# Optimization experiments

Measured on AMD Instinct MI355X. Metric: run time of the kernel, lower is better.

Reference implementation:

```python
import jax, jax.numpy as jnp
import numpy as np
import math

B, N, K, H = 128, 39, 10, 256
RATIO = 0.8
K1 = math.ceil(RATIO * N)    # 32
K2 = math.ceil(RATIO * K1)   # 26
K3 = math.ceil(RATIO * K2)   # 21


def _edge_conv(x_flat, nb, n, w, b):
    # DynamicEdgeConv: per-graph kNN on features (self included, as torch_cluster.knn),
    # message = relu(Linear([x_i, x_j - x_i])), max aggregation over the K neighbors.
    f = x_flat.shape[-1]
    x = x_flat.reshape(nb, n, f)
    sq = jnp.sum(x * x, axis=-1)                                   # [nb,n]
    d = sq[:, :, None] + sq[:, None, :] - 2.0 * jnp.einsum('bif,bjf->bij', x, x)
    _, idx = jax.lax.top_k(-d, K)                                  # [nb,n,K] nearest
    xj = x[jnp.arange(nb)[:, None, None], idx]                     # [nb,n,K,f]
    xi = x[:, :, None, :]
    msg = jnp.concatenate([jnp.broadcast_to(xi, xj.shape), xj - xi], axis=-1)
    h = jax.nn.relu(msg @ w + b)
    return jnp.max(h, axis=2).reshape(nb * n, -1)


def _gcn_score(x_flat, adj, w, b):
    # GCNConv(in,1) with self-loops + symmetric normalization (SAGPool score layer)
    nb, n, _ = adj.shape
    x = x_flat.reshape(nb, n, -1)
    a = adj + jnp.eye(n, dtype=adj.dtype)
    dinv = jax.lax.rsqrt(jnp.sum(a, axis=-1))
    an = a * dinv[:, :, None] * dinv[:, None, :]
    s = jnp.einsum('bij,bjf->bif', an, x @ w) + b
    return s[..., 0]                                               # [nb,n]


def _sag_pool(x_flat, adj, k, w, b):
    # SAGPool: GCN score, per-graph top-k, gate kept nodes by tanh(score), filter adj.
    nb, n, _ = adj.shape
    score = _gcn_score(x_flat, adj, w, b)
    top, loc = jax.lax.top_k(score, k)                             # [nb,k]
    bi = jnp.arange(nb)[:, None]
    x = x_flat.reshape(nb, n, -1)
    xp = x[bi, loc] * jnp.tanh(top)[..., None]
    adj_p = adj[jnp.arange(nb)[:, None, None], loc[:, :, None], loc[:, None, :]]
    perm = (bi * n + loc).reshape(-1)                              # flat node ids
    return xp.reshape(nb * k, -1), adj_p, perm


def _bn(x, g, b, eps=1e-5):
    m = jnp.mean(x, axis=0)
    v = jnp.var(x, axis=0)
    return (x - m) * jax.lax.rsqrt(v + eps) * g + b


def _readout(x_flat, nb, k):
    x = x_flat.reshape(nb, k, -1)
    return jnp.concatenate([jnp.max(x, axis=1), jnp.mean(x, axis=1)], axis=1)


def reference(x, adj, w_mlp1, b_mlp1, w_mlp2, b_mlp2, w_mlp3, b_mlp3, w_mlp6, b_mlp6,
              bn1_g, bn1_b, bn2_g, bn2_b, bn3_g, bn3_b,
              p1_w, p1_b, p2_w, p2_b, p3_w, p3_b,
              lin1_w, lin1_b, lin2_w, lin2_b, lin3_w, lin3_b,
              lin4_w, lin4_b, lin5_w, lin5_b, lin6_w, lin6_b):
    relu = jax.nn.relu
    deg_gt = jnp.sum(adj, axis=-1).reshape(B * N)                  # degree(edge_index[0])

    def decoder(xf):
        d = jnp.tanh(_edge_conv(xf, B, N, w_mlp3, b_mlp3))         # conv4
        d = jnp.tanh(_edge_conv(d, B, N, w_mlp2, b_mlp2))          # conv5
        return _edge_conv(d, B, N, w_mlp6, b_mlp6)                 # conv6

    def degree_head(xf):
        h = relu(xf @ lin4_w + lin4_b)
        h = relu(h @ lin5_w + lin5_b)
        return relu(h @ lin6_w + lin6_b)

    # ---- level 1 ----
    h1 = relu(_bn(_edge_conv(x.reshape(B * N, N), B, N, w_mlp1, b_mlp1), bn1_g, bn1_b))
    xp1, adj1, perm1 = _sag_pool(h1, adj, K1, p1_w, p1_b)
    x_out1 = jnp.zeros_like(h1).at[perm1].set(xp1)
    x_dec1 = decoder(x_out1)
    x_degree = degree_head(x_out1)   # source reuses this tensor for levels 2/3 preds
    gt1, pred1 = deg_gt[perm1], x_degree[perm1]
    r1 = _readout(xp1, B, K1)

    # ---- level 2 ----
    h2 = relu(_bn(_edge_conv(xp1, B, K1, w_mlp2, b_mlp2), bn2_g, bn2_b))
    xp2, adj2, perm2 = _sag_pool(h2, adj1, K2, p2_w, p2_b)
    inner2 = jnp.zeros_like(h2).at[perm2].set(xp2)
    x_out2 = jnp.zeros_like(h1).at[perm1].set(inner2)
    x_dec2 = decoder(x_out2)
    gt2, pred2 = deg_gt[perm2], x_degree[perm2]
    r2 = _readout(xp2, B, K2)

    # ---- level 3 ----
    h3 = relu(_bn(_edge_conv(xp2, B, K2, w_mlp3, b_mlp3), bn3_g, bn3_b))
    xp3, adj3, perm3 = _sag_pool(h3, adj2, K3, p3_w, p3_b)
    inner3 = jnp.zeros_like(h3).at[perm3].set(xp3)
    x_out3 = jnp.zeros_like(h1).at[perm2].set(inner3)  # faithful: source uses perm_2 here
    x_dec3 = decoder(x_out3)
    gt3, pred3 = deg_gt[perm3], x_degree[perm3]
    r3 = _readout(xp3, B, K3)

    z = r1 + r2 + r3
    z = relu(z @ lin1_w + lin1_b)
    z = relu(z @ lin2_w + lin2_b)
    probs = jax.nn.softmax(z @ lin3_w + lin3_b, axis=1)
    return (probs, x_dec1, x_dec2, x_dec3, gt1, pred1, gt2, pred2, gt3, pred3)


def setup_inputs() -> dict:
    key = jax.random.key(0)
    ks = jax.random.split(key, 32)
    rn = lambda i, shape: jax.random.normal(ks[i], shape, dtype=jnp.float32) * 0.05
    x = jax.random.normal(ks[0], (B, N, N), dtype=jnp.float32)
    adj = (jax.random.uniform(ks[1], (B, N, N)) < 0.2).astype(jnp.float32)
    adj = adj * (1.0 - jnp.eye(N, dtype=jnp.float32))
    return dict(
        x=x, adj=adj,
        w_mlp1=rn(2, (2 * N, H)), b_mlp1=rn(3, (H,)),
        w_mlp2=rn(4, (2 * H, H)), b_mlp2=rn(5, (H,)),
        w_mlp3=rn(6, (2 * H, H)), b_mlp3=rn(7, (H,)),
        w_mlp6=rn(8, (2 * H, N)), b_mlp6=rn(9, (N,)),
        bn1_g=jnp.ones((H,), jnp.float32), bn1_b=jnp.zeros((H,), jnp.float32),
        bn2_g=jnp.ones((H,), jnp.float32), bn2_b=jnp.zeros((H,), jnp.float32),
        bn3_g=jnp.ones((H,), jnp.float32), bn3_b=jnp.zeros((H,), jnp.float32),
        p1_w=rn(10, (H, 1)), p1_b=rn(11, (1,)),
        p2_w=rn(12, (H, 1)), p2_b=rn(13, (1,)),
        p3_w=rn(14, (H, 1)), p3_b=rn(15, (1,)),
        lin1_w=rn(16, (2 * H, H)), lin1_b=rn(17, (H,)),
        lin2_w=rn(18, (H, H // 2)), lin2_b=rn(19, (H // 2,)),
        lin3_w=rn(20, (H // 2, 2)), lin3_b=rn(21, (2,)),
        lin4_w=rn(22, (H, H)), lin4_b=rn(23, (H,)),
        lin5_w=rn(24, (H, H // 2)), lin5_b=rn(25, (H // 2,)),
        lin6_w=rn(26, (H // 2, 1)), lin6_b=rn(27, (1,)))
```

## Files before the change

kernel.cpp:

```cpp
#include <hip/hip_runtime.h>
#include <cmath>

#define B_   128
#define N_   39
#define KNN_ 10
#define H_   256
#define K1_  32
#define K2_  26
#define K3_  21

static inline int cdiv(int a, int b) { return (a + b - 1) / b; }

typedef __attribute__((ext_vector_type(8))) short short8;
typedef __attribute__((ext_vector_type(4))) short short4v;
typedef __attribute__((ext_vector_type(4))) float floatx4;

__device__ inline short f2b(float f) {
  unsigned u = __float_as_uint(f);
  u += 0x7fff + ((u >> 16) & 1);
  return (short)(u >> 16);
}
__device__ inline float b2f(short h) {
  return __uint_as_float(((unsigned)(unsigned short)h) << 16);
}
__device__ inline void f2b3(float v, short& h, short& m, short& l) {
  h = f2b(v);
  float r1 = v - b2f(h);
  m = f2b(r1);
  l = f2b(r1 - b2f(m));
}

__global__ void prep_kernel(
    const float* __restrict__ w1, const float* __restrict__ w2,
    const float* __restrict__ w3, const float* __restrict__ w6,
    const float* __restrict__ l4, const float* __restrict__ l5,
    const float* __restrict__ x, const float* __restrict__ adj,
    short* __restrict__ wt1h, short* __restrict__ wt1m, short* __restrict__ wt1l,
    short* __restrict__ wt2h, short* __restrict__ wt2m, short* __restrict__ wt2l,
    short* __restrict__ wt3h, short* __restrict__ wt3m, short* __restrict__ wt3l,
    short* __restrict__ wt6h, short* __restrict__ wt6m,
    short* __restrict__ l4h, short* __restrict__ l4m,
    short* __restrict__ l5h, short* __restrict__ l5m,
    short* __restrict__ xsph, short* __restrict__ xspm, short* __restrict__ xspl,
    float* __restrict__ deg) {
  int task = blockIdx.y;
  int t = blockIdx.x * 256 + threadIdx.x;
  if (task == 0) {
    if (t >= 512 * 64) return;
    int nn = t >> 6, k = t & 63;
    float v = 0.f;
    if (k < 39) v = (nn < 256) ? w1[k * 256 + nn] - w1[(39 + k) * 256 + nn]
                               : w1[(39 + k) * 256 + (nn - 256)];
    short h, m, l; f2b3(v, h, m, l);
    wt1h[t] = h; wt1m[t] = m; wt1l[t] = l;
  } else if (task == 1) {
    if (t >= 512 * 256) return;
    int nn = t >> 8, k = t & 255;
    float v = (nn < 256) ? w2[k * 256 + nn] - w2[(256 + k) * 256 + nn]
                         : w2[(256 + k) * 256 + (nn - 256)];
    short h, m, l; f2b3(v, h, m, l);
    wt2h[t] = h; wt2m[t] = m; wt2l[t] = l;
  } else if (task == 2) {
    if (t >= 512 * 256) return;
    int nn = t >> 8, k = t & 255;
    float v = (nn < 256) ? w3[k * 256 + nn] - w3[(256 + k) * 256 + nn]
                         : w3[(256 + k) * 256 + (nn - 256)];
    short h, m, l; f2b3(v, h, m, l);
    wt3h[t] = h; wt3m[t] = m; wt3l[t] = l;
  } else if (task == 3) {
    if (t >= 78 * 256) return;
    int nn = t >> 8, k = t & 255;
    float v = (nn < 39) ? w6[k * 39 + nn] - w6[(256 + k) * 39 + nn]
                        : w6[(256 + k) * 39 + (nn - 39)];
    short h, m, l; f2b3(v, h, m, l);
    wt6h[t] = h; wt6m[t] = m;
  } else if (task == 4) {
    if (t >= 256 * 256) return;
    int nn = t >> 8, k = t & 255;
    short h, m, l; f2b3(l4[k * 256 + nn], h, m, l);
    l4h[t] = h; l4m[t] = m;
  } else if (task == 5) {
    if (t >= 128 * 256) return;
    int nn = t >> 8, k = t & 255;
    short h, m, l; f2b3(l5[k * 128 + nn], h, m, l);
    l5h[t] = h; l5m[t] = m;
  } else if (task == 6) {
    if (t >= 4992 * 64) return;
    int r = t >> 6, k = t & 63;
    float v = (k < 39) ? x[r * 39 + k] : 0.f;
    short h, m, l; f2b3(v, h, m, l);
    xsph[t] = h; xspm[t] = m; xspl[t] = l;
  } else {
    if (t >= B_ * N_) return;
    const float* row = adj + (size_t)t * N_;
    float s = 0.f;
    for (int j = 0; j < N_; ++j) s += row[j];
    deg[t] = s;
  }
}

__global__ __launch_bounds__(512) void knn_gemm_kernel(
    const short* __restrict__ kxh, const short* __restrict__ kxm, const short* __restrict__ kxl,
    int knt, int kKs, int kn, int kF32, int* __restrict__ idx, int knnB,
    const short* __restrict__ Ah, const short* __restrict__ Am, const short* __restrict__ Al,
    int gnt, int gK,
    const short* __restrict__ Wh, const short* __restrict__ Wm, const short* __restrict__ Wl,
    float* __restrict__ C0, int gM, int gN, int gyB,
    size_t Astride, size_t Cstride) {
  extern __shared__ char smem[];
  int tid = threadIdx.x;
  int wave = tid >> 6, lane = tid & 63;
  int lm = lane & 15, lk = (lane >> 4) * 8;
  if ((int)blockIdx.x < knnB) {
    short* sh_h = (short*)smem;
    short* sh_m = sh_h + 48 * 40;
    short* sh_l = sh_m + 48 * 40;
    float* Gs   = (float*)(sh_l + 48 * 40);
    float* diag = Gs + 48 * 49;
    int b = blockIdx.x;
    int nt = (kn + 15) >> 4;
    int tasks = nt * nt;
    floatx4 acc[2] = {};
    int stage_elems = 384 * knt;
    for (int k0 = 0; k0 < kF32; k0 += 32) {
      for (int e = tid; e < stage_elems; e += 512) {
        int a = e / 384, rem = e - a * 384;
        int r = rem >> 3, c4 = (rem & 7) * 4;
        const short* src = (a == 0) ? kxh : (a == 1) ? kxm : kxl;
        short* dst = (a == 0) ? sh_h : (a == 1) ? sh_m : sh_l;
        *(short4v*)&dst[r * 40 + c4] =
            *(const short4v*)&src[((size_t)(b * kn + r)) * kKs + k0 + c4];
      }
      __syncthreads();
#pragma unroll
      for (int ai = 0; ai < 2; ++ai) {
        int t = wave + ai * 8;
        if (t < tasks) {
          int ti = t / nt, tj = t - ti * nt;
          int ra = (ti * 16 + lm) * 40 + lk;
          int rb = (tj * 16 + lm) * 40 + lk;
          short8 ah = *(const short8*)&sh_h[ra];
          short8 am = *(const short8*)&sh_m[ra];
          short8 bh = *(const short8*)&sh_h[rb];
          short8 bm = *(const short8*)&sh_m[rb];
          floatx4 a = acc[ai];
          a = __builtin_amdgcn_mfma_f32_16x16x32_bf16(ah, bh, a, 0, 0, 0);
          a = __builtin_amdgcn_mfma_f32_16x16x32_bf16(ah, bm, a, 0, 0, 0);
          a = __builtin_amdgcn_mfma_f32_16x16x32_bf16(am, bh, a, 0, 0, 0);
          if (knt == 3) {
            short8 al = *(const short8*)&sh_l[ra];
            short8 bl = *(const short8*)&sh_l[rb];
            a = __builtin_amdgcn_mfma_f32_16x16x32_bf16(ah, bl, a, 0, 0, 0);
            a = __builtin_amdgcn_mfma_f32_16x16x32_bf16(al, bh, a, 0, 0, 0);
            a = __builtin_amdgcn_mfma_f32_16x16x32_bf16(am, bm, a, 0, 0, 0);
          }
          acc[ai] = a;
        }
      }
      __syncthreads();
    }
#pragma unroll
    for (int ai = 0; ai < 2; ++ai) {
      int t = wave + ai * 8;
      if (t < tasks) {
        int ti = t / nt, tj = t - ti * nt;
        int col = tj * 16 + lm;
        int rbase = ti * 16 + (lane >> 4) * 4;
#pragma unroll
        for (int r = 0; r < 4; ++r) Gs[(rbase + r) * 49 + col] = acc[ai][r];
      }
    }
    __syncthreads();
    if (tid < 48) diag[tid] = (tid < kn) ? Gs[tid * 49 + tid] : INFINITY;
    __syncthreads();
    for (int row = wave; row < kn; row += 8) {
      float gii = diag[row];
      float dj = (lane < kn) ? (gii + diag[lane] - 2.f * Gs[row * 49 + lane]) : INFINITY;
      int rank = 0;
      for (int j = 0; j < kn; ++j) {
        float djp = gii + diag[j] - 2.f * Gs[row * 49 + j];
        rank += (djp < dj || (djp == dj && j < lane)) ? 1 : 0;
      }
      if (lane < kn && rank < KNN_)
        idx[(size_t)(b * kn + row) * KNN_ + rank] = lane;
    }
  } else {
    short* Ash = (short*)smem;
    short* Asm = Ash + 128 * 40;
    short* Asl = Asm + 128 * 40;
    short* Bsh = (short*)smem + gnt * 128 * 40;
    short* Bsm = Bsh + 128 * 40;
    short* Bsl = Bsm + 128 * 40;
    int gb = blockIdx.x - knnB;
    int gxB = (gN + 127) >> 7;
    int gx = gb % gxB;
    int rest = gb / gxB;
    int gy = rest % gyB;
    int gz = rest / gyB;
    const short* A_h = Ah + (size_t)gz * Astride;
    const short* A_m = Am ? Am + (size_t)gz * Astride : nullptr;
    const short* A_l = Al ? Al + (size_t)gz * Astride : nullptr;
    float* C = C0 + (size_t)gz * Cstride;
    int row0 = gy * 128, col0 = gx * 128;
    int wm = wave & 1, wn = wave >> 1;
    floatx4 acc[4][2] = {};
    for (int k0 = 0; k0 < gK; k0 += 32) {
      for (int e = tid; e < gnt * 512; e += 512) {
        int a = e >> 9, rem = e & 511;
        int r = rem >> 2, kc = (rem & 3) * 8;
        const short* src = (a == 0) ? A_h : (a == 1) ? A_m : A_l;
        short* dst = (a == 0) ? Ash : (a == 1) ? Asm : Asl;
        *(short8*)&dst[r * 40 + kc] = *(const short8*)&src[((size_t)(row0 + r)) * gK + k0 + kc];
      }
      for (int e = tid; e < gnt * 512; e += 512) {
        int a = e >> 9, rem = e & 511;
        int r = rem >> 2, kc = (rem & 3) * 8;
        const short* src = (a == 0) ? Wh : (a == 1) ? Wm : Wl;
        short* dst = (a == 0) ? Bsh : (a == 1) ? Bsm : Bsl;
        *(short8*)&dst[r * 40 + kc] = *(const short8*)&src[((size_t)(col0 + r)) * gK + k0 + kc];
      }
      __syncthreads();
      short8 afh[4], afm[4], afl[4];
#pragma unroll
      for (int mi = 0; mi < 4; ++mi) {
        int ro = (wm * 64 + mi * 16 + lm) * 40 + lk;
        afh[mi] = *(const short8*)&Ash[ro];
        if (gnt == 3) {
          afm[mi] = *(const short8*)&Asm[ro];
          afl[mi] = *(const short8*)&Asl[ro];
        } else {
          afm[mi] = *(const short8*)&Asm[ro];
        }
      }
#pragma unroll
      for (int ni = 0; ni < 2; ++ni) {
        int ro = (wn * 32 + ni * 16 + lm) * 40 + lk;
        short8 bfh = *(const short8*)&Bsh[ro];
        short8 bfm = *(const short8*)&Bsm[ro];
#pragma unroll
        for (int mi = 0; mi < 4; ++mi) {
          floatx4 a = acc[mi][ni];
          a = __builtin_amdgcn_mfma_f32_16x16x32_bf16(afh[mi], bfh, a, 0, 0, 0);
          a = __builtin_amdgcn_mfma_f32_16x16x32_bf16(afh[mi], bfm, a, 0, 0, 0);
          a = __builtin_amdgcn_mfma_f32_16x16x32_bf16(afm[mi], bfh, a, 0, 0, 0);
          if (gnt == 3) {
            short8 bfl = *(const short8*)&Bsl[ro];
            a = __builtin_amdgcn_mfma_f32_16x16x32_bf16(afh[mi], bfl, a, 0, 0, 0);
            a = __builtin_amdgcn_mfma_f32_16x16x32_bf16(afl[mi], bfh, a, 0, 0, 0);
            a = __builtin_amdgcn_mfma_f32_16x16x32_bf16(afm[mi], bfm, a, 0, 0, 0);
          }
          acc[mi][ni] = a;
        }
      }
      __syncthreads();
    }
    int lr = (lane >> 4) * 4;
#pragma unroll
    for (int mi = 0; mi < 4; ++mi)
#pragma unroll
      for (int ni = 0; ni < 2; ++ni) {
        int colg = col0 + wn * 32 + ni * 16 + lm;
        if (colg >= gN) continue;
#pragma unroll
        for (int r = 0; r < 4; ++r) {
          int rowg = row0 + wm * 64 + mi * 16 + lr + r;
          C[(size_t)rowg * gN + colg] = acc[mi][ni][r];
        }
      }
  }
}

__global__ __launch_bounds__(256) void degree_head_kernel(
    const short* __restrict__ Xh, const short* __restrict__ Xm,
    const short* __restrict__ W4h, const short* __restrict__ W4m, const float* __restrict__ b4,
    const short* __restrict__ W5h, const short* __restrict__ W5m, const float* __restrict__ b5,
    const float* __restrict__ w6, const float* __restrict__ b6,
    float* __restrict__ xdeg) {
  __shared__ __attribute__((aligned(16))) short Ash[32 * 40];
  __shared__ __attribute__((aligned(16))) short Asm[32 * 40];
  __shared__ __attribute__((aligned(16))) short Bsh[256 * 40];
  __shared__ __attribute__((aligned(16))) short Bsm[256 * 40];
  __shared__ __attribute__((aligned(16))) short H1h[32][264];
  __shared__ __attribute__((aligned(16))) short H1m[32][264];
  __shared__ float rowsum[32];
  int tid = threadIdx.x;
  int wave = tid >> 6, lane = tid & 63;
  int lm = lane & 15, g = lane >> 4, lk = g * 8;
  int row0 = blockIdx.x * 32;

  floatx4 acc[2][4] = {};
  for (int k0 = 0; k0 < 256; k0 += 32) {
    {
      int e = tid;
      int a = e >> 7, rem = e & 127;
      int r = rem >> 2, kc = (rem & 3) * 8;
      const short* src = a ? Xm : Xh;
      short* dst = a ? Asm : Ash;
      *(short8*)&dst[r * 40 + kc] = *(const short8*)&src[(size_t)(row0 + r) * 256 + k0 + kc];
    }
#pragma unroll
    for (int i = 0; i < 8; ++i) {
      int e = tid + i * 256;
      int a = e >> 10, rem = e & 1023;
      int r = rem >> 2, kc = (rem & 3) * 8;
      const short* src = a ? W4m : W4h;
      short* dst = a ? Bsm : Bsh;
      *(short8*)&dst[r * 40 + kc] = *(const short8*)&src[(size_t)r * 256 + k0 + kc];
    }
    __syncthreads();
    short8 afh[2], afm[2];
#pragma unroll
    for (int rt = 0; rt < 2; ++rt) {
      int ro = (rt * 16 + lm) * 40 + lk;
      afh[rt] = *(const short8*)&Ash[ro];
      afm[rt] = *(const short8*)&Asm[ro];
    }
#pragma unroll
    for (int ct = 0; ct < 4; ++ct) {
      int ro = (wave * 64 + ct * 16 + lm) * 40 + lk;
      short8 bfh = *(const short8*)&Bsh[ro];
      short8 bfm = *(const short8*)&Bsm[ro];
#pragma unroll
      for (int rt = 0; rt < 2; ++rt) {
        floatx4 a = acc[rt][ct];
        a = __builtin_amdgcn_mfma_f32_16x16x32_bf16(afh[rt], bfh, a, 0, 0, 0);
        a = __builtin_amdgcn_mfma_f32_16x16x32_bf16(afh[rt], bfm, a, 0, 0, 0);
        a = __builtin_amdgcn_mfma_f32_16x16x32_bf16(afm[rt], bfh, a, 0, 0, 0);
        acc[rt][ct] = a;
      }
    }
    __syncthreads();
  }
#pragma unroll
  for (int rt = 0; rt < 2; ++rt)
#pragma unroll
    for (int ct = 0; ct < 4; ++ct) {
      int col = wave * 64 + ct * 16 + lm;
      float bv = b4[col];
#pragma unroll
      for (int r = 0; r < 4; ++r) {
        int row = rt * 16 + g * 4 + r;
        float v = fmaxf(acc[rt][ct][r] + bv, 0.f);
        short hh = f2b(v);
        H1h[row][col] = hh;
        H1m[row][col] = f2b(v - b2f(hh));
      }
    }
  if (tid < 32) rowsum[tid] = 0.f;
  __syncthreads();

  floatx4 acc2[2][2] = {};
  for (int k0 = 0; k0 < 256; k0 += 32) {
#pragma unroll
    for (int i = 0; i < 4; ++i) {
      int e = tid + i * 256;
      int a = e >> 9, rem = e & 511;
      int r = rem >> 2, kc = (rem & 3) * 8;
      const short* src = a ? W5m : W5h;
      short* dst = a ? Bsm : Bsh;
      *(short8*)&dst[r * 40 + kc] = *(const short8*)&src[(size_t)r * 256 + k0 + kc];
    }
    __syncthreads();
    short8 afh[2], afm[2];
#pragma unroll
    for (int rt = 0; rt < 2; ++rt) {
      afh[rt] = *(const short8*)&H1h[rt * 16 + lm][k0 + lk];
      afm[rt] = *(const short8*)&H1m[rt * 16 + lm][k0 + lk];
    }
#pragma unroll
    for (int ct = 0; ct < 2; ++ct) {
      int ro = (wave * 32 + ct * 16 + lm) * 40 + lk;
      short8 bfh = *(const short8*)&Bsh[ro];
      short8 bfm = *(const short8*)&Bsm[ro];
#pragma unroll
      for (int rt = 0; rt < 2; ++rt) {
        floatx4 a = acc2[rt][ct];
        a = __builtin_amdgcn_mfma_f32_16x16x32_bf16(afh[rt], bfh, a, 0, 0, 0);
        a = __builtin_amdgcn_mfma_f32_16x16x32_bf16(afh[rt], bfm, a, 0, 0, 0);
        a = __builtin_amdgcn_mfma_f32_16x16x32_bf16(afm[rt], bfh, a, 0, 0, 0);
        acc2[rt][ct] = a;
      }
    }
    __syncthreads();
  }

#pragma unroll
  for (int rt = 0; rt < 2; ++rt) {
#pragma unroll
    for (int r = 0; r < 4; ++r) {
      float p = 0.f;
#pragma unroll
      for (int ct = 0; ct < 2; ++ct) {
        int col = wave * 32 + ct * 16 + lm;
        float v = fmaxf(acc2[rt][ct][r] + b5[col], 0.f);
        p += v * w6[col];
      }
#pragma unroll
      for (int off = 1; off < 16; off <<= 1) p += __shfl_xor(p, off, 64);
      if (lm == 0) atomicAdd(&rowsum[rt * 16 + g * 4 + r], p);
    }
  }
  __syncthreads();
  if (tid < 32) xdeg[row0 + tid] = fmaxf(rowsum[tid] + b6[0], 0.f);
}

__global__ __launch_bounds__(256) void rowgemm_kernel(
    const float* __restrict__ A, const float* __restrict__ W, const float* __restrict__ bias,
    float* __restrict__ C, int N, int K, int act) {
  __shared__ float a[512];
  int row = blockIdx.x;
  for (int k = threadIdx.x; k < K; k += 256) a[k] = A[(size_t)row * K + k];
  __syncthreads();
  for (int c = threadIdx.x; c < N; c += 256) {
    float s = 0.f;
    for (int k = 0; k < K; k += 4) {
      float4 av = *(const float4*)&a[k];
      s += av.x * W[(size_t)k * N + c];
      s += av.y * W[(size_t)(k + 1) * N + c];
      s += av.z * W[(size_t)(k + 2) * N + c];
      s += av.w * W[(size_t)(k + 3) * N + c];
    }
    float v = s + (bias ? bias[c] : 0.f);
    if (act == 1) v = fmaxf(v, 0.f);
    C[(size_t)row * N + c] = v;
  }
}

__global__ void wavedot_gemm_kernel(const float* __restrict__ A, const float* __restrict__ W,
                                    const float* __restrict__ bias, float* __restrict__ C,
                                    int M, int N, int K, int act) {
  int wid = (blockIdx.x * blockDim.x + threadIdx.x) >> 6;
  int lane = threadIdx.x & 63;
  if (wid >= M * N) return;
  int row = wid / N, col = wid - row * N;
  const float* ar = A + (size_t)row * K;
  float s = 0.f;
  for (int k = lane; k < K; k += 64) s += ar[k] * W[(size_t)k * N + col];
  for (int off = 32; off; off >>= 1) s += __shfl_down(s, off, 64);
  if (lane == 0) {
    float v = s + (bias ? bias[col] : 0.f);
    if (act == 1) v = fmaxf(v, 0.f);
    C[(size_t)row * N + col] = v;
  }
}

__global__ void edge_agg_kernel(const float* __restrict__ AB, const float* __restrict__ bias,
                                const int* __restrict__ idx, int n, int Hc, int act,
                                int rows, int per,
                                float* __restrict__ out,
                                short* __restrict__ outh, short* __restrict__ outm,
                                short* __restrict__ outl) {
  int t = blockIdx.x * blockDim.x + threadIdx.x;
  if (t >= rows * Hc) return;
  int r = t / Hc, h = t - r * Hc;
  int d = r / per, rloc = r - d * per;
  int b = rloc / n;
  int s2 = 2 * Hc;
  float av = AB[(size_t)r * s2 + h] + bias[h];
  const int* ir = idx + ((size_t)d * per + rloc) * KNN_;
  int base = d * per + b * n;
  float m = -INFINITY;
  for (int k = 0; k < KNN_; ++k) {
    float v = av + AB[(size_t)(base + ir[k]) * s2 + Hc + h];
    v = fmaxf(v, 0.f);
    m = fmaxf(m, v);
  }
  if (act == 2) m = tanhf(m);
  if (out) out[t] = m;
  if (outh) {
    short hh, mm, ll;
    f2b3(m, hh, mm, ll);
    outh[t] = hh; outm[t] = mm;
    if (outl) outl[t] = ll;
  }
}

__global__ void bn_stats_kernel(const float* __restrict__ xx, int M,
                                const float* __restrict__ g, const float* __restrict__ bb,
                                float* __restrict__ scsh) {
  int c = blockIdx.x;
  double s = 0.0, s2 = 0.0;
  for (int r = threadIdx.x; r < M; r += 256) {
    double v = (double)xx[(size_t)r * H_ + c];
    s += v; s2 += v * v;
  }
  __shared__ double sh[256], sh2[256];
  sh[threadIdx.x] = s; sh2[threadIdx.x] = s2;
  __syncthreads();
  for (int o = 128; o; o >>= 1) {
    if (threadIdx.x < o) { sh[threadIdx.x] += sh[threadIdx.x + o]; sh2[threadIdx.x] += sh2[threadIdx.x + o]; }
    __syncthreads();
  }
  if (threadIdx.x == 0) {
    double mean = sh[0] / M;
    double var = sh2[0] / M - mean * mean;
    float rstd = 1.f / sqrtf((float)var + 1e-5f);
    float sc = rstd * g[c];
    scsh[c] = sc;
    scsh[H_ + c] = bb[c] - (float)mean * sc;
  }
}

__global__ void bnrowdot_kernel(const float* __restrict__ t1, const float* __restrict__ scsh,
                                const float* __restrict__ pw, int M, float* __restrict__ ys) {
  int wid = (blockIdx.x * blockDim.x + threadIdx.x) >> 6;
  int lane = threadIdx.x & 63;
  if (wid >= M) return;
  const float* xr = t1 + (size_t)wid * H_;
  float s = 0.f;
  for (int k = lane; k < H_; k += 64) {
    float v = fmaxf(xr[k] * scsh[k] + scsh[H_ + k], 0.f);
    s += v * pw[k];
  }
  for (int off = 32; off; off >>= 1) s += __shfl_down(s, off, 64);
  if (lane == 0) ys[wid] = s;
}

__global__ __launch_bounds__(256) void sag_select_kernel(
    const float* __restrict__ ysg,
    const float* __restrict__ adj_in, int n, int k,
    const float* __restrict__ pb,
    int* __restrict__ perm, float* __restrict__ tantg, int* __restrict__ locsg,
    float* __restrict__ adjp,
    const float* __restrict__ deg, const float* __restrict__ xdeg,
    float* __restrict__ gt, float* __restrict__ pred) {
  __shared__ float ys[40], dinv[40], scs[40];
  __shared__ int locs[40];
  int b = blockIdx.x;
  int i = threadIdx.x;
  if (i < n) {
    ys[i] = ysg[b * n + i];
    const float* ar = adj_in + ((size_t)b * n + i) * n;
    float sum = 1.f;
    for (int j = 0; j < n; ++j) sum += ar[j];
    dinv[i] = 1.f / sqrtf(sum);
  }
  __syncthreads();
  if (i < n) {
    const float* ar = adj_in + ((size_t)b * n + i) * n;
    float acc = 0.f;
    for (int j = 0; j < n; ++j) {
      float a = ar[j] + (i == j ? 1.f : 0.f);
      acc += a * dinv[j] * ys[j];
    }
    scs[i] = dinv[i] * acc + pb[0];
  }
  __syncthreads();
  if (i < n) {
    float si = scs[i];
    int rank = 0;
    for (int j = 0; j < n; ++j) {
      float sj = scs[j];
      rank += (sj > si || (sj == si && j < i)) ? 1 : 0;
    }
    if (rank < k) {
      tantg[b * k + rank] = tanhf(si);
      locsg[b * k + rank] = i;
      locs[rank] = i;
      perm[b * k + rank] = b * n + i;
    }
  }
  __syncthreads();
  if (adjp) {
    for (int e = threadIdx.x; e < k * k; e += 256) {
      int t1i = e / k, t2i = e - t1i * k;
      adjp[(size_t)b * k * k + e] = adj_in[((size_t)b * n + locs[t1i]) * n + locs[t2i]];
    }
  }
  if (gt && threadIdx.x < k) {
    int p = b * n + locs[threadIdx.x];
    gt[b * k + threadIdx.x] = deg[p];
    pred[b * k + threadIdx.x] = xdeg[p];
  }
}

__global__ void pool_scatter_kernel(
    const float* __restrict__ t1, const float* __restrict__ scsh,
    const float* __restrict__ tantg, const int* __restrict__ locsg,
    const int* __restrict__ remap, int n, int k,
    short* __restrict__ xph, short* __restrict__ xpm, short* __restrict__ xpl,
    short* __restrict__ soh, short* __restrict__ som) {
  int t = blockIdx.x * blockDim.x + threadIdx.x;
  if (t >= B_ * k * H_) return;
  int r = t >> 8, hc = t & 255;
  int b = r / k, rr = r - b * k;
  int own = b * n + locsg[b * k + rr];
  float v = fmaxf(t1[(size_t)own * H_ + hc] * scsh[hc] + scsh[H_ + hc], 0.f) * tantg[b * k + rr];
  short hh, mm, ll;
  f2b3(v, hh, mm, ll);
  xph[t] = hh; xpm[t] = mm; xpl[t] = ll;
  int tgt = remap ? remap[own] : own;
  size_t so = (size_t)tgt * H_ + hc;
  soh[so] = hh; som[so] = mm;
}

__global__ void readout_kernel(const short* __restrict__ xph, const short* __restrict__ xpm,
                               const short* __restrict__ xpl, int k, int accum,
                               float* __restrict__ z) {
  int t = blockIdx.x * blockDim.x + threadIdx.x;
  if (t >= B_ * H_) return;
  int b = t >> 8, hc = t & 255;
  float mx = -INFINITY, sm = 0.f;
  for (int r = 0; r < k; ++r) {
    size_t o = ((size_t)(b * k + r)) * H_ + hc;
    float v = b2f(xph[o]) + b2f(xpm[o]) + b2f(xpl[o]);
    mx = fmaxf(mx, v);
    sm += v;
  }
  float* zb = z + (size_t)b * 2 * H_;
  float mean = sm / (float)k;
  if (accum) { zb[hc] += mx; zb[H_ + hc] += mean; }
  else       { zb[hc] = mx;  zb[H_ + hc] = mean; }
}

__global__ void gtpred_kernel(const float* __restrict__ deg, const float* __restrict__ xdeg,
                              const int* __restrict__ perm, int M,
                              float* __restrict__ gt, float* __restrict__ pred) {
  int t = blockIdx.x * blockDim.x + threadIdx.x;
  if (t >= M) return;
  int p = perm[t];
  gt[t] = deg[p];
  pred[t] = xdeg[p];
}

__global__ void softmax2_kernel(const float* __restrict__ logits, float* __restrict__ probs) {
  int b = blockIdx.x * blockDim.x + threadIdx.x;
  if (b >= B_) return;
  float a = logits[2 * b], c = logits[2 * b + 1];
  float m = fmaxf(a, c);
  float ea = expf(a - m), ec = expf(c - m);
  float inv = 1.f / (ea + ec);
  probs[2 * b] = ea * inv;
  probs[2 * b + 1] = ec * inv;
}

extern "C" void kernel_launch(void* const* d_in, const int* in_sizes, int n_in,
                              void* d_out, int out_size, void* d_ws, size_t ws_size,
                              hipStream_t stream) {
  auto in = [&](int i) { return (const float*)d_in[i]; };
  const float* x      = in(0);
  const float* adj    = in(1);
  const float* w_mlp1 = in(2);  const float* b_mlp1 = in(3);
  const float* w_mlp2 = in(4);  const float* b_mlp2 = in(5);
  const float* w_mlp3 = in(6);  const float* b_mlp3 = in(7);
  const float* w_mlp6 = in(8);  const float* b_mlp6 = in(9);
  const float* bn1_g = in(10);  const float* bn1_b = in(11);
  const float* bn2_g = in(12);  const float* bn2_b = in(13);
  const float* bn3_g = in(14);  const float* bn3_b = in(15);
  const float* p1_w = in(16);   const float* p1_b = in(17);
  const float* p2_w = in(18);   const float* p2_b = in(19);
  const float* p3_w = in(20);   const float* p3_b = in(21);
  const float* lin1_w = in(22); const float* lin1_b = in(23);
  const float* lin2_w = in(24); const float* lin2_b = in(25);
  const float* lin3_w = in(26); const float* lin3_b = in(27);
  const float* lin4_w = in(28); const float* lin4_b = in(29);
  const float* lin5_w = in(30); const float* lin5_b = in(31);
  const float* lin6_w = in(32); const float* lin6_b = in(33);

  float* out = (float*)d_out;
  float* out_probs = out;
  float* out_dec1  = out_probs + 256;
  float* out_gt1   = out_dec1 + 3 * 4992 * 39;
  float* out_pred1 = out_gt1 + 4096;
  float* out_gt2   = out_pred1 + 4096;
  float* out_pred2 = out_gt2 + 3328;
  float* out_gt3   = out_pred2 + 3328;
  float* out_pred3 = out_gt3 + 2688;

  char* base = (char*)d_ws;
  size_t off = 0;
  auto allocf = [&](size_t n) -> float* {
    float* p = (float*)(base + off);
    off += ((n * sizeof(float) + 255) & ~(size_t)255);
    return p;
  };
  auto alloci = [&](size_t n) -> int* {
    int* p = (int*)(base + off);
    off += ((n * sizeof(int) + 255) & ~(size_t)255);
    return p;
  };
  auto allocs = [&](size_t n) -> short* {
    short* p = (short*)(base + off);
    off += ((n * sizeof(short) + 255) & ~(size_t)255);
    return p;
  };

  const size_t S = (size_t)4992 * 256;
  const size_t AB_S = (size_t)4992 * 512;
  const int SI = 4992 * KNN_;

  short* wt1h = allocs(512 * 64); short* wt1m = allocs(512 * 64); short* wt1l = allocs(512 * 64);
  short* wt2h = allocs(512 * 256); short* wt2m = allocs(512 * 256); short* wt2l = allocs(512 * 256);
  short* wt3h = allocs(512 * 256); short* wt3m = allocs(512 * 256); short* wt3l = allocs(512 * 256);
  short* wt6h = allocs(78 * 256);  short* wt6m = allocs(78 * 256);
  short* l4h = allocs(256 * 256);  short* l4m = allocs(256 * 256);
  short* l5h = allocs(128 * 256);  short* l5m = allocs(128 * 256);
  short* xsph = allocs(4992 * 64); short* xspm = allocs(4992 * 64); short* xspl = allocs(4992 * 64);
  float* deg  = allocf(4992);
  float* xdeg = allocf(4992);
  float* ysg  = allocf(4992);
  int* idxb = alloci(3 * SI);
  float* AB3 = allocf(3 * AB_S);
  float* trunk_t1 = allocf(S);
  float* scsh = allocf(512);
  float* tantg = allocf(4096);
  int* locsg = alloci(4096);
  short* xph = allocs((size_t)4096 * 256); short* xpm = allocs((size_t)4096 * 256); short* xpl = allocs((size_t)4096 * 256);
  size_t ms0 = off;
  short* xoutb_h = allocs(3 * S);
  short* xoutb_m = allocs(3 * S);
  size_t msz = off - ms0;
  short* t1b_h = allocs(3 * S);
  short* t1b_m = allocs(3 * S);
  float* adj1 = allocf(128 * 32 * 32);
  float* adj2 = allocf(128 * 26 * 26);
  int* perm1 = alloci(4096); int* perm2 = alloci(3328); int* perm3 = alloci(2688);
  float* z  = allocf(128 * 512);
  float* z1 = allocf(128 * 256);
  float* z2 = allocf(128 * 128);
  float* logits = allocf(256);
  if (off > ws_size) return;

  short* t2b_h = xoutb_h; short* t2b_m = xoutb_m;

  const size_t LDS3 = 6 * 128 * 40 * sizeof(short);
  const size_t LDS2 = 4 * 128 * 40 * sizeof(short);

  prep_kernel<<<dim3(1248, 8), 256, 0, stream>>>(
      w_mlp1, w_mlp2, w_mlp3, w_mlp6, lin4_w, lin5_w, x, adj,
      wt1h, wt1m, wt1l, wt2h, wt2m, wt2l, wt3h, wt3m, wt3l, wt6h, wt6m,
      l4h, l4m, l5h, l5m, xsph, xspm, xspl, deg);
  hipMemsetAsync(xoutb_h, 0, msz, stream);

  knn_gemm_kernel<<<B_ + 4 * 39, 512, LDS3, stream>>>(
      xsph, xspm, xspl, 3, 64, N_, 64, idxb, B_,
      xsph, xspm, xspl, 3, 64, wt1h, wt1m, wt1l, AB3, 4992, 512, 39, 0, 0);
  edge_agg_kernel<<<cdiv(4992 * 256, 256), 256, 0, stream>>>(AB3, b_mlp1, idxb, N_, 256, 0, 4992, 4992,
                                                             trunk_t1, nullptr, nullptr, nullptr);
  bn_stats_kernel<<<H_, 256, 0, stream>>>(trunk_t1, 4992, bn1_g, bn1_b, scsh);
  bnrowdot_kernel<<<cdiv(4992 * 64, 256), 256, 0, stream>>>(trunk_t1, scsh, p1_w, 4992, ysg);
  sag_select_kernel<<<B_, 256, 0, stream>>>(ysg, adj, N_, K1_, p1_b,
                                            perm1, tantg, locsg, adj1,
                                            nullptr, nullptr, nullptr, nullptr);
  pool_scatter_kernel<<<cdiv(B_ * K1_ * H_, 256), 256, 0, stream>>>(
      trunk_t1, scsh, tantg, locsg, nullptr, N_, K1_, xph, xpm, xpl, xoutb_h, xoutb_m);
  readout_kernel<<<cdiv(B_ * H_, 256), 256, 0, stream>>>(xph, xpm, xpl, K1_, 0, z);
  degree_head_kernel<<<156, 256, 0, stream>>>(
      xoutb_h, xoutb_m, l4h, l4m, lin4_b, l5h, l5m, lin5_b, lin6_w, lin6_b, xdeg);
  gtpred_kernel<<<cdiv(4096, 256), 256, 0, stream>>>(deg, xdeg, perm1, 4096, out_gt1, out_pred1);

  knn_gemm_kernel<<<B_ + 4 * 32, 512, LDS3, stream>>>(
      xph, xpm, xpl, 3, 256, K1_, 256, idxb, B_,
      xph, xpm, xpl, 3, 256, wt2h, wt2m, wt2l, AB3, 4096, 512, 32, 0, 0);
  edge_agg_kernel<<<cdiv(4096 * 256, 256), 256, 0, stream>>>(AB3, b_mlp2, idxb, K1_, 256, 0, 4096, 4096,
                                                             trunk_t1, nullptr, nullptr, nullptr);
  bn_stats_kernel<<<H_, 256, 0, stream>>>(trunk_t1, 4096, bn2_g, bn2_b, scsh);
  bnrowdot_kernel<<<cdiv(4096 * 64, 256), 256, 0, stream>>>(trunk_t1, scsh, p2_w, 4096, ysg);
  sag_select_kernel<<<B_, 256, 0, stream>>>(ysg, adj1, K1_, K2_, p2_b,
                                            perm2, tantg, locsg, adj2,
                                            deg, xdeg, out_gt2, out_pred2);
  pool_scatter_kernel<<<cdiv(B_ * K2_ * H_, 256), 256, 0, stream>>>(
      trunk_t1, scsh, tantg, locsg, perm1, K1_, K2_, xph, xpm, xpl, xoutb_h + S, xoutb_m + S);
  readout_kernel<<<cdiv(B_ * H_, 256), 256, 0, stream>>>(xph, xpm, xpl, K2_, 1, z);

  knn_gemm_kernel<<<B_ + 4 * 26, 512, LDS3, stream>>>(
      xph, xpm, xpl, 3, 256, K2_, 256, idxb, B_,
      xph, xpm, xpl, 3, 256, wt3h, wt3m, wt3l, AB3, 3328, 512, 26, 0, 0);
  edge_agg_kernel<<<cdiv(3328 * 256, 256), 256, 0, stream>>>(AB3, b_mlp3, idxb, K2_, 256, 0, 3328, 3328,
                                                             trunk_t1, nullptr, nullptr, nullptr);
  bn_stats_kernel<<<H_, 256, 0, stream>>>(trunk_t1, 3328, bn3_g, bn3_b, scsh);
  bnrowdot_kernel<<<cdiv(3328 * 64, 256), 256, 0, stream>>>(trunk_t1, scsh, p3_w, 3328, ysg);
  sag_select_kernel<<<B_, 256, 0, stream>>>(ysg, adj2, K2_, K3_, p3_b,
                                            perm3, tantg, locsg, nullptr,
                                            deg, xdeg, out_gt3, out_pred3);
  pool_scatter_kernel<<<cdiv(B_ * K3_ * H_, 256), 256, 0, stream>>>(
      trunk_t1, scsh, tantg, locsg, perm2, K2_, K3_, xph, xpm, xpl, xoutb_h + 2 * S, xoutb_m + 2 * S);
  readout_kernel<<<cdiv(B_ * H_, 256), 256, 0, stream>>>(xph, xpm, xpl, K3_, 1, z);

  rowgemm_kernel<<<128, 256, 0, stream>>>(z, lin1_w, lin1_b, z1, 256, 512, 1);
  rowgemm_kernel<<<128, 256, 0, stream>>>(z1, lin2_w, lin2_b, z2, 128, 256, 1);
  wavedot_gemm_kernel<<<cdiv(128 * 2 * 64, 256), 256, 0, stream>>>(z2, lin3_w, lin3_b, logits, 128, 2, 128, 0);
  softmax2_kernel<<<1, 128, 0, stream>>>(logits, out_probs);

  knn_gemm_kernel<<<3 * B_ + 4 * 39 * 3, 512, LDS2, stream>>>(
      xoutb_h, xoutb_m, nullptr, 2, 256, N_, 256, idxb, 3 * B_,
      xoutb_h, xoutb_m, nullptr, 2, 256, wt3h, wt3m, nullptr, AB3, 4992, 512, 39, S, AB_S);
  edge_agg_kernel<<<cdiv(3 * 4992 * 256, 256), 256, 0, stream>>>(
      AB3, b_mlp3, idxb, N_, 256, 2, 3 * 4992, 4992, nullptr, t1b_h, t1b_m, nullptr);
  knn_gemm_kernel<<<3 * B_ + 4 * 39 * 3, 512, LDS2, stream>>>(
      t1b_h, t1b_m, nullptr, 2, 256, N_, 256, idxb, 3 * B_,
      t1b_h, t1b_m, nullptr, 2, 256, wt2h, wt2m, nullptr, AB3, 4992, 512, 39, S, AB_S);
  edge_agg_kernel<<<cdiv(3 * 4992 * 256, 256), 256, 0, stream>>>(
      AB3, b_mlp2, idxb, N_, 256, 2, 3 * 4992, 4992, nullptr, t2b_h, t2b_m, nullptr);
  knn_gemm_kernel<<<3 * B_ + 1 * 39 * 3, 512, LDS2, stream>>>(
      t2b_h, t2b_m, nullptr, 2, 256, N_, 256, idxb, 3 * B_,
      t2b_h, t2b_m, nullptr, 2, 256, wt6h, wt6m, nullptr, AB3, 4992, 78, 39, S, (size_t)4992 * 78);
  edge_agg_kernel<<<cdiv(3 * 4992 * 39, 256), 256, 0, stream>>>(
      AB3, b_mlp6, idxb, N_, 39, 0, 3 * 4992, 4992, out_dec1, nullptr, nullptr, nullptr);
}
```

Before: 521.8 us.

## Fuse kNN, edge GEMM and max aggregation into one per-graph-tile kernel

Replaces the separate kNN/GEMM kernel and edge aggregation kernel with one kernel. Each block handles a group of whole graphs and a 128-column slice of interleaved weights, and computes the Gram matrix, the kNN ranks and the edge messages with their max in LDS. This removes the large fp32 AB intermediate round-trip to global memory and the idx buffer. The SAG score row-dot is folded into sag_select, and pool_scatter and readout are merged into a single kernel. In exchange, each column block recomputes the kNN (4x redundant), and the larger LDS footprint may lower occupancy.

```diff
diff --git a/kernel.cpp b/kernel.cpp
--- a/kernel.cpp
+++ b/kernel.cpp
@@ -99,174 +99,214 @@
   }
 }
 
-__global__ __launch_bounds__(512) void knn_gemm_kernel(
-    const short* __restrict__ kxh, const short* __restrict__ kxm, const short* __restrict__ kxl,
-    int knt, int kKs, int kn, int kF32, int* __restrict__ idx, int knnB,
-    const short* __restrict__ Ah, const short* __restrict__ Am, const short* __restrict__ Al,
-    int gnt, int gK,
+__global__ __launch_bounds__(512) void gemmagg_kernel(
+    const short* __restrict__ Xh, const short* __restrict__ Xm, const short* __restrict__ Xl,
     const short* __restrict__ Wh, const short* __restrict__ Wm, const short* __restrict__ Wl,
-    float* __restrict__ C0, int gM, int gN, int gyB,
-    size_t Astride, size_t Cstride) {
+    const float* __restrict__ bias, int Kdim, int n, int G, int nGraphs, int mode,
+    short* __restrict__ Oh, short* __restrict__ Om, float* __restrict__ Ofp) {
   extern __shared__ char smem[];
+  const int nt = Xl ? 3 : 2;
+  short* Ash = (short*)smem;
+  short* Asm = Ash + 5120;
+  short* Asl = Asm + 5120;
+  short* Bsh = (short*)smem + nt * 5120;
+  short* Bsm = Bsh + 5120;
+  short* Bsl = Bsm + 5120;
+  float* Cs  = (float*)smem;
+  float* Gm  = (float*)smem;
+  int*   idxl = (int*)(smem + 66560);
+  float* sBias = (float*)(smem + 71680);
+  float* diag  = (float*)(smem + 72704);
   int tid = threadIdx.x;
   int wave = tid >> 6, lane = tid & 63;
-  int lm = lane & 15, lk = (lane >> 4) * 8;
-  if ((int)blockIdx.x < knnB) {
-    short* sh_h = (short*)smem;
-    short* sh_m = sh_h + 48 * 40;
-    short* sh_l = sh_m + 48 * 40;
-    float* Gs   = (float*)(sh_l + 48 * 40);
-    float* diag = Gs + 48 * 49;
-    int b = blockIdx.x;
-    int nt = (kn + 15) >> 4;
-    int tasks = nt * nt;
-    floatx4 acc[2] = {};
-    int stage_elems = 384 * knt;
-    for (int k0 = 0; k0 < kF32; k0 += 32) {
-      for (int e = tid; e < stage_elems; e += 512) {
-        int a = e / 384, rem = e - a * 384;
-        int r = rem >> 3, c4 = (rem & 7) * 4;
-        const short* src = (a == 0) ? kxh : (a == 1) ? kxm : kxl;
-        short* dst = (a == 0) ? sh_h : (a == 1) ? sh_m : sh_l;
-        *(short4v*)&dst[r * 40 + c4] =
-            *(const short4v*)&src[((size_t)(b * kn + r)) * kKs + k0 + c4];
-      }
-      __syncthreads();
-#pragma unroll
-      for (int ai = 0; ai < 2; ++ai) {
-        int t = wave + ai * 8;
-        if (t < tasks) {
-          int ti = t / nt, tj = t - ti * nt;
-          int ra = (ti * 16 + lm) * 40 + lk;
-          int rb = (tj * 16 + lm) * 40 + lk;
-          short8 ah = *(const short8*)&sh_h[ra];
-          short8 am = *(const short8*)&sh_m[ra];
-          short8 bh = *(const short8*)&sh_h[rb];
-          short8 bm = *(const short8*)&sh_m[rb];
-          floatx4 a = acc[ai];
-          a = __builtin_amdgcn_mfma_f32_16x16x32_bf16(ah, bh, a, 0, 0, 0);
-          a = __builtin_amdgcn_mfma_f32_16x16x32_bf16(ah, bm, a, 0, 0, 0);
-          a = __builtin_amdgcn_mfma_f32_16x16x32_bf16(am, bh, a, 0, 0, 0);
-          if (knt == 3) {
-            short8 al = *(const short8*)&sh_l[ra];
-            short8 bl = *(const short8*)&sh_l[rb];
-            a = __builtin_amdgcn_mfma_f32_16x16x32_bf16(ah, bl, a, 0, 0, 0);
-            a = __builtin_amdgcn_mfma_f32_16x16x32_bf16(al, bh, a, 0, 0, 0);
-            a = __builtin_amdgcn_mfma_f32_16x16x32_bf16(am, bm, a, 0, 0, 0);
-          }
-          acc[ai] = a;
-        }
-      }
-      __syncthreads();
-    }
-#pragma unroll
-    for (int ai = 0; ai < 2; ++ai) {
+  int lm = lane & 15, lg = lane >> 4, lk = lg * 8;
+  int gx = blockIdx.x, gy = blockIdx.y;
+  int col0 = gx * 128;
+  int g0 = gy * G;
+  int gcount = min(G, nGraphs - g0);
+  int rows = gcount * n;
+  size_t row0g = (size_t)g0 * n;
+  int ntt = (n + 15) >> 4;
+  int tpg = ntt * ntt;
+  int tasks = gcount * tpg;
+  int nA = (mode == 2) ? 39 : 256;
+
+  for (int e = tid; e < nA; e += 512) sBias[e] = bias[e];
+
+  int raOff[4], rbOff[4];
+#pragma unroll
+  for (int ai = 0; ai < 4; ++ai) {
+    int t = wave + ai * 8;
+    if (t < tasks) {
+      int gl = t / tpg, tt = t - gl * tpg;
+      int ti = tt / ntt, tj = tt - ti * ntt;
+      raOff[ai] = (gl * n + ti * 16 + lm) * 40 + lk;
+      rbOff[ai] = (gl * n + tj * 16 + lm) * 40 + lk;
+    } else { raOff[ai] = 0; rbOff[ai] = 0; }
+  }
+
+  int wm = wave & 1, wn = wave >> 1;
+  floatx4 acc[4][2] = {};
+  floatx4 accg[4] = {};
+  for (int k0 = 0; k0 < Kdim; k0 += 32) {
+    for (int e = tid; e < nt * 512; e += 512) {
+      int a = e >> 9, rem = e & 511;
+      int r = rem >> 2, kc = (rem & 3) * 8;
+      const short* src = (a == 0) ? Xh : (a == 1) ? Xm : Xl;
+      short* dst = (a == 0) ? Ash : (a == 1) ? Asm : Asl;
+      short8 v = {};
+      if (r < rows) v = *(const short8*)&src[(row0g + r) * Kdim + k0 + kc];
+      *(short8*)&dst[r * 40 + kc] = v;
+    }
+    for (int e = tid; e < nt * 512; e += 512) {
+      int a = e >> 9, rem = e & 511;
+      int r = rem >> 2, kc = (rem & 3) * 8;
+      const short* src = (a == 0) ? Wh : (a == 1) ? Wm : Wl;
+      short* dst = (a == 0) ? Bsh : (a == 1) ? Bsm : Bsl;
+      int p = col0 + r;
+      short8 v = {};
+      if (p < 2 * nA) {
+        int wr = (p >> 1) + (p & 1) * nA;
+        v = *(const short8*)&src[(size_t)wr * Kdim + k0 + kc];
+      }
+      *(short8*)&dst[r * 40 + kc] = v;
+    }
+    __syncthreads();
+#pragma unroll
+    for (int ai = 0; ai < 4; ++ai) {
       int t = wave + ai * 8;
       if (t < tasks) {
-        int ti = t / nt, tj = t - ti * nt;
-        int col = tj * 16 + lm;
-        int rbase = ti * 16 + (lane >> 4) * 4;
-#pragma unroll
-        for (int r = 0; r < 4; ++r) Gs[(rbase + r) * 49 + col] = acc[ai][r];
+        short8 ah = *(const short8*)&Ash[raOff[ai]];
+        short8 am = *(const short8*)&Asm[raOff[ai]];
+        short8 bh = *(const short8*)&Ash[rbOff[ai]];
+        short8 bm = *(const short8*)&Asm[rbOff[ai]];
+        floatx4 a = accg[ai];
+        a = __builtin_amdgcn_mfma_f32_16x16x32_bf16(ah, bh, a, 0, 0, 0);
+        a = __builtin_amdgcn_mfma_f32_16x16x32_bf16(ah, bm, a, 0, 0, 0);
+        a = __builtin_amdgcn_mfma_f32_16x16x32_bf16(am, bh, a, 0, 0, 0);
+        if (nt == 3) {
+          short8 al = *(const short8*)&Asl[raOff[ai]];
+          short8 bl = *(const short8*)&Asl[rbOff[ai]];
+          a = __builtin_amdgcn_mfma_f32_16x16x32_bf16(ah, bl, a, 0, 0, 0);
+          a = __builtin_amdgcn_mfma_f32_16x16x32_bf16(al, bh, a, 0, 0, 0);
+          a = __builtin_amdgcn_mfma_f32_16x16x32_bf16(am, bm, a, 0, 0, 0);
+        }
+        accg[ai] = a;
+      }
+    }
+    short8 afh[4], afm[4], afl[4];
+#pragma unroll
+    for (int mi = 0; mi < 4; ++mi) {
+      int ro = (wm * 64 + mi * 16 + lm) * 40 + lk;
+      afh[mi] = *(const short8*)&Ash[ro];
+      afm[mi] = *(const short8*)&Asm[ro];
+      if (nt == 3) afl[mi] = *(const short8*)&Asl[ro];
+    }
+#pragma unroll
+    for (int ni = 0; ni < 2; ++ni) {
+      int ro = (wn * 32 + ni * 16 + lm) * 40 + lk;
+      short8 bfh = *(const short8*)&Bsh[ro];
+      short8 bfm = *(const short8*)&Bsm[ro];
+#pragma unroll
+      for (int mi = 0; mi < 4; ++mi) {
+        floatx4 a = acc[mi][ni];
+        a = __builtin_amdgcn_mfma_f32_16x16x32_bf16(afh[mi], bfh, a, 0, 0, 0);
+        a = __builtin_amdgcn_mfma_f32_16x16x32_bf16(afh[mi], bfm, a, 0, 0, 0);
+        a = __builtin_amdgcn_mfma_f32_16x16x32_bf16(afm[mi], bfh, a, 0, 0, 0);
+        if (nt == 3) {
+          short8 bfl = *(const short8*)&Bsl[ro];
+          a = __builtin_amdgcn_mfma_f32_16x16x32_bf16(afh[mi], bfl, a, 0, 0, 0);
+          a = __builtin_amdgcn_mfma_f32_16x16x32_bf16(afl[mi], bfh, a, 0, 0, 0);
+          a = __builtin_amdgcn_mfma_f32_16x16x32_bf16(afm[mi], bfm, a, 0, 0, 0);
+        }
+        acc[mi][ni] = a;
       }
     }
     __syncthreads();
-    if (tid < 48) diag[tid] = (tid < kn) ? Gs[tid * 49 + tid] : INFINITY;
-    __syncthreads();
-    for (int row = wave; row < kn; row += 8) {
-      float gii = diag[row];
-      float dj = (lane < kn) ? (gii + diag[lane] - 2.f * Gs[row * 49 + lane]) : INFINITY;
-      int rank = 0;
-      for (int j = 0; j < kn; ++j) {
-        float djp = gii + diag[j] - 2.f * Gs[row * 49 + j];
-        rank += (djp < dj || (djp == dj && j < lane)) ? 1 : 0;
-      }
-      if (lane < kn && rank < KNN_)
-        idx[(size_t)(b * kn + row) * KNN_ + rank] = lane;
+  }
+
+#pragma unroll
+  for (int ai = 0; ai < 4; ++ai) {
+    int t = wave + ai * 8;
+    if (t < tasks) {
+      int gl = t / tpg, tt = t - gl * tpg;
+      int ti = tt / ntt, tj = tt - ti * ntt;
+      int col = tj * 16 + lm;
+      if (col < n) {
+        int rbase = ti * 16 + lg * 4;
+#pragma unroll
+        for (int r = 0; r < 4; ++r) {
+          int row = rbase + r;
+          if (row < n) Gm[(gl * n + row) * (n + 1) + col] = accg[ai][r];
+        }
+      }
+    }
+  }
+  __syncthreads();
+  for (int rr = tid; rr < rows; rr += 512) diag[rr] = Gm[rr * (n + 1) + (rr % n)];
+  __syncthreads();
+  for (int rr = wave; rr < rows; rr += 8) {
+    float gii = diag[rr];
+    int gb = (rr / n) * n;
+    float dj = (lane < n) ? (gii + diag[gb + lane] - 2.f * Gm[rr * (n + 1) + lane]) : INFINITY;
+    int rank = 0;
+    for (int j = 0; j < n; ++j) {
+      float djp = gii + diag[gb + j] - 2.f * Gm[rr * (n + 1) + j];
+      rank += (djp < dj || (djp == dj && j < lane)) ? 1 : 0;
+    }
+    if (lane < n && rank < KNN_) idxl[rr * KNN_ + rank] = lane;
+  }
+  __syncthreads();
+  int lr = lg * 4;
+#pragma unroll
+  for (int mi = 0; mi < 4; ++mi)
+#pragma unroll
+    for (int ni = 0; ni < 2; ++ni) {
+      int col = wn * 32 + ni * 16 + lm;
+#pragma unroll
+      for (int r = 0; r < 4; ++r) {
+        int row = wm * 64 + mi * 16 + lr + r;
+        Cs[row * 130 + col] = acc[mi][ni][r];
+      }
+    }
+  __syncthreads();
+  if (mode == 2) {
+    for (int e = tid; e < rows * 39; e += 512) {
+      int r = e / 39, h = e - r * 39;
+      float av = Cs[r * 130 + 2 * h] + sBias[h];
+      int gb = (r / n) * n;
+      const int* ir = &idxl[r * KNN_];
+      float mx = -INFINITY;
+#pragma unroll
+      for (int k = 0; k < KNN_; ++k) {
+        float v = fmaxf(av + Cs[(gb + ir[k]) * 130 + 2 * h + 1], 0.f);
+        mx = fmaxf(mx, v);
+      }
+      Ofp[(row0g + r) * 39 + h] = mx;
     }
   } else {
-    short* Ash = (short*)smem;
-    short* Asm = Ash + 128 * 40;
-    short* Asl = Asm + 128 * 40;
-    short* Bsh = (short*)smem + gnt * 128 * 40;
-    short* Bsm = Bsh + 128 * 40;
-    short* Bsl = Bsm + 128 * 40;
-    int gb = blockIdx.x - knnB;
-    int gxB = (gN + 127) >> 7;
-    int gx = gb % gxB;
-    int rest = gb / gxB;
-    int gy = rest % gyB;
-    int gz = rest / gyB;
-    const short* A_h = Ah + (size_t)gz * Astride;
-    const short* A_m = Am ? Am + (size_t)gz * Astride : nullptr;
-    const short* A_l = Al ? Al + (size_t)gz * Astride : nullptr;
-    float* C = C0 + (size_t)gz * Cstride;
-    int row0 = gy * 128, col0 = gx * 128;
-    int wm = wave & 1, wn = wave >> 1;
-    floatx4 acc[4][2] = {};
-    for (int k0 = 0; k0 < gK; k0 += 32) {
-      for (int e = tid; e < gnt * 512; e += 512) {
-        int a = e >> 9, rem = e & 511;
-        int r = rem >> 2, kc = (rem & 3) * 8;
-        const short* src = (a == 0) ? A_h : (a == 1) ? A_m : A_l;
-        short* dst = (a == 0) ? Ash : (a == 1) ? Asm : Asl;
-        *(short8*)&dst[r * 40 + kc] = *(const short8*)&src[((size_t)(row0 + r)) * gK + k0 + kc];
-      }
-      for (int e = tid; e < gnt * 512; e += 512) {
-        int a = e >> 9, rem = e & 511;
-        int r = rem >> 2, kc = (rem & 3) * 8;
-        const short* src = (a == 0) ? Wh : (a == 1) ? Wm : Wl;
-        short* dst = (a == 0) ? Bsh : (a == 1) ? Bsm : Bsl;
-        *(short8*)&dst[r * 40 + kc] = *(const short8*)&src[((size_t)(col0 + r)) * gK + k0 + kc];
-      }
-      __syncthreads();
-      short8 afh[4], afm[4], afl[4];
-#pragma unroll
-      for (int mi = 0; mi < 4; ++mi) {
-        int ro = (wm * 64 + mi * 16 + lm) * 40 + lk;
-        afh[mi] = *(const short8*)&Ash[ro];
-        if (gnt == 3) {
-          afm[mi] = *(const short8*)&Asm[ro];
-          afl[mi] = *(const short8*)&Asl[ro];
-        } else {
-          afm[mi] = *(const short8*)&Asm[ro];
-        }
-      }
-#pragma unroll
-      for (int ni = 0; ni < 2; ++ni) {
-        int ro = (wn * 32 + ni * 16 + lm) * 40 + lk;
-        short8 bfh = *(const short8*)&Bsh[ro];
-        short8 bfm = *(const short8*)&Bsm[ro];
-#pragma unroll
-        for (int mi = 0; mi < 4; ++mi) {
-          floatx4 a = acc[mi][ni];
-          a = __builtin_amdgcn_mfma_f32_16x16x32_bf16(afh[mi], bfh, a, 0, 0, 0);
-          a = __builtin_amdgcn_mfma_f32_16x16x32_bf16(afh[mi], bfm, a, 0, 0, 0);
-          a = __builtin_amdgcn_mfma_f32_16x16x32_bf16(afm[mi], bfh, a, 0, 0, 0);
-          if (gnt == 3) {
-            short8 bfl = *(const short8*)&Bsl[ro];
-            a = __builtin_amdgcn_mfma_f32_16x16x32_bf16(afh[mi], bfl, a, 0, 0, 0);
-            a = __builtin_amdgcn_mfma_f32_16x16x32_bf16(afl[mi], bfh, a, 0, 0, 0);
-            a = __builtin_amdgcn_mfma_f32_16x16x32_bf16(afm[mi], bfm, a, 0, 0, 0);
-          }
-          acc[mi][ni] = a;
-        }
-      }
-      __syncthreads();
-    }
-    int lr = (lane >> 4) * 4;
-#pragma unroll
-    for (int mi = 0; mi < 4; ++mi)
-#pragma unroll
-      for (int ni = 0; ni < 2; ++ni) {
-        int colg = col0 + wn * 32 + ni * 16 + lm;
-        if (colg >= gN) continue;
-#pragma unroll
-        for (int r = 0; r < 4; ++r) {
-          int rowg = row0 + wm * 64 + mi * 16 + lr + r;
-          C[(size_t)rowg * gN + colg] = acc[mi][ni][r];
-        }
-      }
+    for (int e = tid; e < rows * 64; e += 512) {
+      int r = e >> 6, h = e & 63;
+      int hg = gx * 64 + h;
+      float av = Cs[r * 130 + 2 * h] + sBias[hg];
+      int gb = (r / n) * n;
+      const int* ir = &idxl[r * KNN_];
+      float mx = -INFINITY;
+#pragma unroll
+      for (int k = 0; k < KNN_; ++k) {
+        float v = fmaxf(av + Cs[(gb + ir[k]) * 130 + 2 * h + 1], 0.f);
+        mx = fmaxf(mx, v);
+      }
+      if (mode == 0) {
+        Ofp[(row0g + r) * 256 + hg] = mx;
+      } else {
+        mx = tanhf(mx);
+        short hh = f2b(mx);
+        short mm2 = f2b(mx - b2f(hh));
+        size_t o = (row0g + r) * 256 + hg;
+        Oh[o] = hh; Om[o] = mm2;
+      }
+    }
   }
 }
 
@@ -383,7 +423,6 @@
     }
     __syncthreads();
   }
-
 #pragma unroll
   for (int rt = 0; rt < 2; ++rt) {
 #pragma unroll
@@ -444,37 +483,6 @@
   }
 }
 
-__global__ void edge_agg_kernel(const float* __restrict__ AB, const float* __restrict__ bias,
-                                const int* __restrict__ idx, int n, int Hc, int act,
-                                int rows, int per,
-                                float* __restrict__ out,
-                                short* __restrict__ outh, short* __restrict__ outm,
-                                short* __restrict__ outl) {
-  int t = blockIdx.x * blockDim.x + threadIdx.x;
-  if (t >= rows * Hc) return;
-  int r = t / Hc, h = t - r * Hc;
-  int d = r / per, rloc = r - d * per;
-  int b = rloc / n;
-  int s2 = 2 * Hc;
-  float av = AB[(size_t)r * s2 + h] + bias[h];
-  const int* ir = idx + ((size_t)d * per + rloc) * KNN_;
-  int base = d * per + b * n;
-  float m = -INFINITY;
-  for (int k = 0; k < KNN_; ++k) {
-    float v = av + AB[(size_t)(base + ir[k]) * s2 + Hc + h];
-    v = fmaxf(v, 0.f);
-    m = fmaxf(m, v);
-  }
-  if (act == 2) m = tanhf(m);
-  if (out) out[t] = m;
-  if (outh) {
-    short hh, mm, ll;
-    f2b3(m, hh, mm, ll);
-    outh[t] = hh; outm[t] = mm;
-    if (outl) outl[t] = ll;
-  }
-}
-
 __global__ void bn_stats_kernel(const float* __restrict__ xx, int M,
                                 const float* __restrict__ g, const float* __restrict__ bb,
                                 float* __restrict__ scsh) {
@@ -501,23 +509,8 @@
   }
 }
 
-__global__ void bnrowdot_kernel(const float* __restrict__ t1, const float* __restrict__ scsh,
-                                const float* __restrict__ pw, int M, float* __restrict__ ys) {
-  int wid = (blockIdx.x * blockDim.x + threadIdx.x) >> 6;
-  int lane = threadIdx.x & 63;
-  if (wid >= M) return;
-  const float* xr = t1 + (size_t)wid * H_;
-  float s = 0.f;
-  for (int k = lane; k < H_; k += 64) {
-    float v = fmaxf(xr[k] * scsh[k] + scsh[H_ + k], 0.f);
-    s += v * pw[k];
-  }
-  for (int off = 32; off; off >>= 1) s += __shfl_down(s, off, 64);
-  if (lane == 0) ys[wid] = s;
-}
-
 __global__ __launch_bounds__(256) void sag_select_kernel(
-    const float* __restrict__ ysg,
+    const float* __restrict__ t1, const float* __restrict__ scsh, const float* __restrict__ pw,
     const float* __restrict__ adj_in, int n, int k,
     const float* __restrict__ pb,
     int* __restrict__ perm, float* __restrict__ tantg, int* __restrict__ locsg,
@@ -528,8 +521,19 @@
   __shared__ int locs[40];
   int b = blockIdx.x;
   int i = threadIdx.x;
+  int wave = i >> 6, lane = i & 63;
+  for (int row = wave; row < n; row += 4) {
+    const float* xr = t1 + (size_t)(b * n + row) * H_;
+    float s = 0.f;
+    for (int kk = lane; kk < H_; kk += 64) {
+      float v = fmaxf(xr[kk] * scsh[kk] + scsh[H_ + kk], 0.f);
+      s += v * pw[kk];
+    }
+    for (int off = 32; off; off >>= 1) s += __shfl_down(s, off, 64);
+    if (lane == 0) ys[row] = s;
+  }
+  __syncthreads();
   if (i < n) {
-    ys[i] = ysg[b * n + i];
     const float* ar = adj_in + ((size_t)b * n + i) * n;
     float sum = 1.f;
     for (int j = 0; j < n; ++j) sum += ar[j];
@@ -574,38 +578,31 @@
   }
 }
 
-__global__ void pool_scatter_kernel(
+__global__ __launch_bounds__(256) void pool_readout_kernel(
     const float* __restrict__ t1, const float* __restrict__ scsh,
     const float* __restrict__ tantg, const int* __restrict__ locsg,
-    const int* __restrict__ remap, int n, int k,
+    const int* __restrict__ remap, int n, int k, int accum,
     short* __restrict__ xph, short* __restrict__ xpm, short* __restrict__ xpl,
-    short* __restrict__ soh, short* __restrict__ som) {
-  int t = blockIdx.x * blockDim.x + threadIdx.x;
-  if (t >= B_ * k * H_) return;
-  int r = t >> 8, hc = t & 255;
-  int b = r / k, rr = r - b * k;
-  int own = b * n + locsg[b * k + rr];
-  float v = fmaxf(t1[(size_t)own * H_ + hc] * scsh[hc] + scsh[H_ + hc], 0.f) * tantg[b * k + rr];
-  short hh, mm, ll;
-  f2b3(v, hh, mm, ll);
-  xph[t] = hh; xpm[t] = mm; xpl[t] = ll;
-  int tgt = remap ? remap[own] : own;
-  size_t so = (size_t)tgt * H_ + hc;
-  soh[so] = hh; som[so] = mm;
-}
-
-__global__ void readout_kernel(const short* __restrict__ xph, const short* __restrict__ xpm,
-                               const short* __restrict__ xpl, int k, int accum,
-                               float* __restrict__ z) {
-  int t = blockIdx.x * blockDim.x + threadIdx.x;
-  if (t >= B_ * H_) return;
-  int b = t >> 8, hc = t & 255;
+    short* __restrict__ soh, short* __restrict__ som, float* __restrict__ z) {
+  int b = blockIdx.x;
+  int hc = threadIdx.x;
+  float sc = scsh[hc], sh = scsh[H_ + hc];
   float mx = -INFINITY, sm = 0.f;
   for (int r = 0; r < k; ++r) {
-    size_t o = ((size_t)(b * k + r)) * H_ + hc;
-    float v = b2f(xph[o]) + b2f(xpm[o]) + b2f(xpl[o]);
-    mx = fmaxf(mx, v);
-    sm += v;
+    int loc = locsg[b * k + r];
+    float tg = tantg[b * k + r];
+    int own = b * n + loc;
+    float v = fmaxf(t1[(size_t)own * H_ + hc] * sc + sh, 0.f) * tg;
+    short hh, mm, ll;
+    f2b3(v, hh, mm, ll);
+    size_t xo = ((size_t)(b * k + r)) * H_ + hc;
+    xph[xo] = hh; xpm[xo] = mm; xpl[xo] = ll;
+    int tgt = remap ? remap[own] : own;
+    size_t so = (size_t)tgt * H_ + hc;
+    soh[so] = hh; som[so] = mm;
+    float vq = b2f(hh) + b2f(mm) + b2f(ll);
+    mx = fmaxf(mx, vq);
+    sm += vq;
   }
   float* zb = z + (size_t)b * 2 * H_;
   float mean = sm / (float)k;
@@ -686,8 +683,6 @@
   };
 
   const size_t S = (size_t)4992 * 256;
-  const size_t AB_S = (size_t)4992 * 512;
-  const int SI = 4992 * KNN_;
 
   short* wt1h = allocs(512 * 64); short* wt1m = allocs(512 * 64); short* wt1l = allocs(512 * 64);
   short* wt2h = allocs(512 * 256); short* wt2m = allocs(512 * 256); short* wt2l = allocs(512 * 256);
@@ -698,9 +693,6 @@
   short* xsph = allocs(4992 * 64); short* xspm = allocs(4992 * 64); short* xspl = allocs(4992 * 64);
   float* deg  = allocf(4992);
   float* xdeg = allocf(4992);
-  float* ysg  = allocf(4992);
-  int* idxb = alloci(3 * SI);
-  float* AB3 = allocf(3 * AB_S);
   float* trunk_t1 = allocf(S);
   float* scsh = allocf(512);
   float* tantg = allocf(4096);
@@ -723,8 +715,13 @@
 
   short* t2b_h = xoutb_h; short* t2b_m = xoutb_m;
 
-  const size_t LDS3 = 6 * 128 * 40 * sizeof(short);
-  const size_t LDS2 = 4 * 128 * 40 * sizeof(short);
+  const size_t GG_LDS = 73216;
+  static int gg_set = 0;
+  if (!gg_set) {
+    hipFuncSetAttribute(reinterpret_cast<const void*>(gemmagg_kernel),
+                        hipFuncAttributeMaxDynamicSharedMemorySize, (int)GG_LDS);
+    gg_set = 1;
+  }
 
   prep_kernel<<<dim3(1248, 8), 256, 0, stream>>>(
       w_mlp1, w_mlp2, w_mlp3, w_mlp6, lin4_w, lin5_w, x, adj,
@@ -732,69 +729,51 @@
       l4h, l4m, l5h, l5m, xsph, xspm, xspl, deg);
   hipMemsetAsync(xoutb_h, 0, msz, stream);
 
-  knn_gemm_kernel<<<B_ + 4 * 39, 512, LDS3, stream>>>(
-      xsph, xspm, xspl, 3, 64, N_, 64, idxb, B_,
-      xsph, xspm, xspl, 3, 64, wt1h, wt1m, wt1l, AB3, 4992, 512, 39, 0, 0);
-  edge_agg_kernel<<<cdiv(4992 * 256, 256), 256, 0, stream>>>(AB3, b_mlp1, idxb, N_, 256, 0, 4992, 4992,
-                                                             trunk_t1, nullptr, nullptr, nullptr);
+  gemmagg_kernel<<<dim3(4, 43), 512, GG_LDS, stream>>>(
+      xsph, xspm, xspl, wt1h, wt1m, wt1l, b_mlp1, 64, 39, 3, 128, 0,
+      nullptr, nullptr, trunk_t1);
   bn_stats_kernel<<<H_, 256, 0, stream>>>(trunk_t1, 4992, bn1_g, bn1_b, scsh);
-  bnrowdot_kernel<<<cdiv(4992 * 64, 256), 256, 0, stream>>>(trunk_t1, scsh, p1_w, 4992, ysg);
-  sag_select_kernel<<<B_, 256, 0, stream>>>(ysg, adj, N_, K1_, p1_b,
+  sag_select_kernel<<<B_, 256, 0, stream>>>(trunk_t1, scsh, p1_w, adj, N_, K1_, p1_b,
                                             perm1, tantg, locsg, adj1,
                                             nullptr, nullptr, nullptr, nullptr);
-  pool_scatter_kernel<<<cdiv(B_ * K1_ * H_, 256), 256, 0, stream>>>(
-      trunk_t1, scsh, tantg, locsg, nullptr, N_, K1_, xph, xpm, xpl, xoutb_h, xoutb_m);
-  readout_kernel<<<cdiv(B_ * H_, 256), 256, 0, stream>>>(xph, xpm, xpl, K1_, 0, z);
+  pool_readout_kernel<<<B_, 256, 0, stream>>>(
+      trunk_t1, scsh, tantg, locsg, nullptr, N_, K1_, 0, xph, xpm, xpl, xoutb_h, xoutb_m, z);
   degree_head_kernel<<<156, 256, 0, stream>>>(
       xoutb_h, xoutb_m, l4h, l4m, lin4_b, l5h, l5m, lin5_b, lin6_w, lin6_b, xdeg);
   gtpred_kernel<<<cdiv(4096, 256), 256, 0, stream>>>(deg, xdeg, perm1, 4096, out_gt1, out_pred1);
 
-  knn_gemm_kernel<<<B_ + 4 * 32, 512, LDS3, stream>>>(
-      xph, xpm, xpl, 3, 256, K1_, 256, idxb, B_,
-      xph, xpm, xpl, 3, 256, wt2h, wt2m, wt2l, AB3, 4096, 512, 32, 0, 0);
-  edge_agg_kernel<<<cdiv(4096 * 256, 256), 256, 0, stream>>>(AB3, b_mlp2, idxb, K1_, 256, 0, 4096, 4096,
-                                                             trunk_t1, nullptr, nullptr, nullptr);
+  gemmagg_kernel<<<dim3(4, 32), 512, GG_LDS, stream>>>(
+      xph, xpm, xpl, wt2h, wt2m, wt2l, b_mlp2, 256, 32, 4, 128, 0,
+      nullptr, nullptr, trunk_t1);
   bn_stats_kernel<<<H_, 256, 0, stream>>>(trunk_t1, 4096, bn2_g, bn2_b, scsh);
-  bnrowdot_kernel<<<cdiv(4096 * 64, 256), 256, 0, stream>>>(trunk_t1, scsh, p2_w, 4096, ysg);
-  sag_select_kernel<<<B_, 256, 0, stream>>>(ysg, adj1, K1_, K2_, p2_b,
+  sag_select_kernel<<<B_, 256, 0, stream>>>(trunk_t1, scsh, p2_w, adj1, K1_, K2_, p2_b,
                                             perm2, tantg, locsg, adj2,
                                             deg, xdeg, out_gt2, out_pred2);
-  pool_scatter_kernel<<<cdiv(B_ * K2_ * H_, 256), 256, 0, stream>>>(
-      trunk_t1, scsh, tantg, locsg, perm1, K1_, K2_, xph, xpm, xpl, xoutb_h + S, xoutb_m + S);
-  readout_kernel<<<cdiv(B_ * H_, 256), 256, 0, stream>>>(xph, xpm, xpl, K2_, 1, z);
-
-  knn_gemm_kernel<<<B_ + 4 * 26, 512, LDS3, stream>>>(
-      xph, xpm, xpl, 3, 256, K2_, 256, idxb, B_,
-      xph, xpm, xpl, 3, 256, wt3h, wt3m, wt3l, AB3, 3328, 512, 26, 0, 0);
-  edge_agg_kernel<<<cdiv(3328 * 256, 256), 256, 0, stream>>>(AB3, b_mlp3, idxb, K2_, 256, 0, 3328, 3328,
-                                                             trunk_t1, nullptr, nullptr, nullptr);
+  pool_readout_kernel<<<B_, 256, 0, stream>>>(
+      trunk_t1, scsh, tantg, locsg, perm1, K1_, K2_, 1, xph, xpm, xpl, xoutb_h + S, xoutb_m + S, z);
+
+  gemmagg_kernel<<<dim3(4, 32), 512, GG_LDS, stream>>>(
+      xph, xpm, xpl, wt3h, wt3m, wt3l, b_mlp3, 256, 26, 4, 128, 0,
+      nullptr, nullptr, trunk_t1);
   bn_stats_kernel<<<H_, 256, 0, stream>>>(trunk_t1, 3328, bn3_g, bn3_b, scsh);
-  bnrowdot_kernel<<<cdiv(3328 * 64, 256), 256, 0, stream>>>(trunk_t1, scsh, p3_w, 3328, ysg);
-  sag_select_kernel<<<B_, 256, 0, stream>>>(ysg, adj2, K2_, K3_, p3_b,
+  sag_select_kernel<<<B_, 256, 0, stream>>>(trunk_t1, scsh, p3_w, adj2, K2_, K3_, p3_b,
                                             perm3, tantg, locsg, nullptr,
                                             deg, xdeg, out_gt3, out_pred3);
-  pool_scatter_kernel<<<cdiv(B_ * K3_ * H_, 256), 256, 0, stream>>>(
-      trunk_t1, scsh, tantg, locsg, perm2, K2_, K3_, xph, xpm, xpl, xoutb_h + 2 * S, xoutb_m + 2 * S);
-  readout_kernel<<<cdiv(B_ * H_, 256), 256, 0, stream>>>(xph, xpm, xpl, K3_, 1, z);
+  pool_readout_kernel<<<B_, 256, 0, stream>>>(
+      trunk_t1, scsh, tantg, locsg, perm2, K2_, K3_, 1, xph, xpm, xpl, xoutb_h + 2 * S, xoutb_m + 2 * S, z);
 
   rowgemm_kernel<<<128, 256, 0, stream>>>(z, lin1_w, lin1_b, z1, 256, 512, 1);
   rowgemm_kernel<<<128, 256, 0, stream>>>(z1, lin2_w, lin2_b, z2, 128, 256, 1);
   wavedot_gemm_kernel<<<cdiv(128 * 2 * 64, 256), 256, 0, stream>>>(z2, lin3_w, lin3_b, logits, 128, 2, 128, 0);
   softmax2_kernel<<<1, 128, 0, stream>>>(logits, out_probs);
 
-  knn_gemm_kernel<<<3 * B_ + 4 * 39 * 3, 512, LDS2, stream>>>(
-      xoutb_h, xoutb_m, nullptr, 2, 256, N_, 256, idxb, 3 * B_,
-      xoutb_h, xoutb_m, nullptr, 2, 256, wt3h, wt3m, nullptr, AB3, 4992, 512, 39, S, AB_S);
-  edge_agg_kernel<<<cdiv(3 * 4992 * 256, 256), 256, 0, stream>>>(
-      AB3, b_mlp3, idxb, N_, 256, 2, 3 * 4992, 4992, nullptr, t1b_h, t1b_m, nullptr);
-  knn_gemm_kernel<<<3 * B_ + 4 * 39 * 3, 512, LDS2, stream>>>(
-      t1b_h, t1b_m, nullptr, 2, 256, N_, 256, idxb, 3 * B_,
-      t1b_h, t1b_m, nullptr, 2, 256, wt2h, wt2m, nullptr, AB3, 4992, 512, 39, S, AB_S);
-  edge_agg_kernel<<<cdiv(3 * 4992 * 256, 256), 256, 0, stream>>>(
-      AB3, b_mlp2, idxb, N_, 256, 2, 3 * 4992, 4992, nullptr, t2b_h, t2b_m, nullptr);
-  knn_gemm_kernel<<<3 * B_ + 1 * 39 * 3, 512, LDS2, stream>>>(
-      t2b_h, t2b_m, nullptr, 2, 256, N_, 256, idxb, 3 * B_,
-      t2b_h, t2b_m, nullptr, 2, 256, wt6h, wt6m, nullptr, AB3, 4992, 78, 39, S, (size_t)4992 * 78);
-  edge_agg_kernel<<<cdiv(3 * 4992 * 39, 256), 256, 0, stream>>>(
-      AB3, b_mlp6, idxb, N_, 39, 0, 3 * 4992, 4992, out_dec1, nullptr, nullptr, nullptr);
-}
+  gemmagg_kernel<<<dim3(4, 128), 512, GG_LDS, stream>>>(
+      xoutb_h, xoutb_m, nullptr, wt3h, wt3m, nullptr, b_mlp3, 256, 39, 3, 384, 1,
+      t1b_h, t1b_m, nullptr);
+  gemmagg_kernel<<<dim3(4, 128), 512, GG_LDS, stream>>>(
+      t1b_h, t1b_m, nullptr, wt2h, wt2m, nullptr, b_mlp2, 256, 39, 3, 384, 1,
+      t2b_h, t2b_m, nullptr);
+  gemmagg_kernel<<<dim3(1, 128), 512, GG_LDS, stream>>>(
+      t2b_h, t2b_m, nullptr, wt6h, wt6m, nullptr, b_mlp6, 256, 39, 3, 384, 2,
+      nullptr, nullptr, out_dec1);
+}
```

Result: slower. 710.2 us (+36.1%).
